# Kernel tuning notes

Hardware: AMD Instinct MI355X
Metric: run time of the kernel (lower is better)

## Reference

```python
import jax, jax.numpy as jnp
import numpy as np
import math

SEQ = 2048      # seq_length_per_batch_item
BATCH = 2
HEADS = 16
HEAD_DIM = 128
SEG_LEN = 1024  # two packed segments per batch item
CAUSAL = True
SCALE = 1.0 / math.sqrt(HEAD_DIM)
MASK_FILL = -10000.0  # matches masked_fill value in torch masked softmax


def setup_inputs() -> dict:
    key = jax.random.key(0)
    k1, k2, k3, k4 = jax.random.split(key, 4)
    query = jax.random.normal(k1, (SEQ, BATCH, HEADS, HEAD_DIM), dtype=jnp.float32)
    key_t = jax.random.normal(k2, (SEQ, BATCH, HEADS, HEAD_DIM), dtype=jnp.float32)
    value = jax.random.normal(k3, (SEQ, BATCH, HEADS, HEAD_DIM), dtype=jnp.float32)
    # additive score manipulation (log-additive branch), broadcast over heads
    score_bias = jax.random.normal(k4, (BATCH, 1, SEQ, SEQ), dtype=jnp.float32) * 0.05
    # packed segment boundaries over the flattened (b*s) token axis;
    # every batch-item boundary (multiple of SEQ) is included, per the torch assert
    cumulative_seq_lengths = jnp.arange(BATCH * SEQ // SEG_LEN + 1, dtype=jnp.int32) * SEG_LEN
    return {
        "query": query,
        "key": key_t,
        "value": value,
        "score_bias": score_bias,
        "cumulative_seq_lengths": cumulative_seq_lengths,
    }


def _dense_mask(cumulative_seq_lengths, batch, seq, causal):
    """Block-diagonal (packed varlen) attention mask.

    Returns bool [b, 1, s, s]; True = masked (disallowed), matching
    cumulative_seq_lengths_to_dense_attention_mask (which returns ~mask).
    """
    # segment id of each token in the flattened (b*s) stream
    flat_pos = jnp.arange(batch * seq, dtype=jnp.int32)
    seg = jnp.searchsorted(cumulative_seq_lengths, flat_pos, side="right")  # [b*s]
    seg = seg.reshape(batch, seq)
    allowed = seg[:, :, None] == seg[:, None, :]  # [b, s, s]
    if causal:
        pos = jnp.arange(seq)
        allowed = allowed & (pos[:, None] >= pos[None, :])
    return ~allowed[:, None, :, :]  # [b, 1, s, s]


def reference(query, key, value, score_bias, cumulative_seq_lengths):
    s, b, n, h = query.shape
    # scores: QK^T scaled -> [b, n, s_q, s_k]
    scores = jnp.einsum("sbnh,tbnh->bnst", query, key) * SCALE
    # additive score manipulation (log-additive branch)
    scores = scores + score_bias
    # block-diagonal varlen mask + causal
    mask = _dense_mask(cumulative_seq_lengths, b, s, CAUSAL)
    scores = jnp.where(mask, MASK_FILL, scores)
    probs = jax.nn.softmax(scores, axis=-1)  # [b, n, s, s]
    # context: probs @ V -> [(b n), s, h], matching torch bmm output layout
    ctx = jnp.einsum("bnst,tbnh->bnsh", probs, value)
    return ctx.reshape(b * n, s, h)
```

## Files before the change

kernel.cpp:

```cpp
#include <hip/hip_runtime.h>
#include <hip/hip_bf16.h>

#define SEQ     2048
#define BATCH   2
#define HEADS   16
#define HD      128
#define SEGL    1024
#define QSCALE  0.08838834764831845f

typedef __attribute__((ext_vector_type(8))) short bf16x8;
typedef __attribute__((ext_vector_type(4))) float f32x4;
typedef unsigned int u32;

__device__ __forceinline__ short f2bf(float f) {
    __hip_bfloat16 h = __float2bfloat16(f);
    return *reinterpret_cast<short*>(&h);
}

__device__ __forceinline__ bf16x8 cvt8(f32x4 x, f32x4 y) {
    bf16x8 t;
    t[0]=f2bf(x[0]); t[1]=f2bf(x[1]); t[2]=f2bf(x[2]); t[3]=f2bf(x[3]);
    t[4]=f2bf(y[0]); t[5]=f2bf(y[1]); t[6]=f2bf(y[2]); t[7]=f2bf(y[3]);
    return t;
}

__device__ __forceinline__ void async16(void* lds, const void* g) {
    __builtin_amdgcn_global_load_lds(
        (const __attribute__((address_space(1))) u32*)g,
        (__attribute__((address_space(3))) u32*)lds, 16, 0, 0);
}

__launch_bounds__(256)
__global__ void prep_kernel(const float* __restrict__ K, const float* __restrict__ V,
                            short* __restrict__ KbfSw, short* __restrict__ VtSw)
{
    const int t  = threadIdx.x;
    const int sT = blockIdx.x;
    const int bh = blockIdx.y;
    const int b  = bh >> 4, h = bh & 15;
    const size_t inBase  = (size_t)sT * 64 * 4096 + (size_t)b * HEADS * HD + (size_t)h * HD;
    const size_t region  = ((size_t)bh * 32 + sT) * 8192;

    if (blockIdx.z == 0) {
        #pragma unroll
        for (int i = 0; i < 4; ++i) {
            const int idx = i * 256 + t;
            const int s_loc = idx >> 4, dg = idx & 15;
            const float* p = K + inBase + (size_t)s_loc * 4096 + dg * 8;
            f32x4 x = *(const f32x4*)p;
            f32x4 y = *(const f32x4*)(p + 4);
            *(bf16x8*)(KbfSw + region + s_loc * 128 + ((dg ^ (s_loc & 7)) * 8)) = cvt8(x, y);
        }
    } else {
        __shared__ __align__(16) short lds[64][136];
        #pragma unroll
        for (int i = 0; i < 4; ++i) {
            const int idx = i * 256 + t;
            const int s_loc = idx >> 4, dg = idx & 15;
            const float* p = V + inBase + (size_t)s_loc * 4096 + dg * 8;
            f32x4 x = *(const f32x4*)p;
            f32x4 y = *(const f32x4*)(p + 4);
            *(bf16x8*)(&lds[s_loc][dg * 8]) = cvt8(x, y);
        }
        __syncthreads();
        const int dp = t & 63;
        const int g  = t >> 6;
        bf16x8 a0, a1, b0_, b1_;
        #pragma unroll
        for (int j = 0; j < 8; ++j) {
            u32 v = *(const u32*)&lds[g * 16 + j][dp * 2];
            a0[j] = (short)(v & 0xffff);
            a1[j] = (short)(v >> 16);
        }
        #pragma unroll
        for (int j = 0; j < 8; ++j) {
            u32 v = *(const u32*)&lds[g * 16 + 8 + j][dp * 2];
            b0_[j] = (short)(v & 0xffff);
            b1_[j] = (short)(v >> 16);
        }
        const int d0c = dp * 2, d1c = dp * 2 + 1;
        short* base0 = VtSw + region + d0c * 64;
        short* base1 = VtSw + region + d1c * 64;
        *(bf16x8*)(base0 + (((g * 2)     ^ (d0c & 7)) * 8)) = a0;
        *(bf16x8*)(base0 + (((g * 2 + 1) ^ (d0c & 7)) * 8)) = b0_;
        *(bf16x8*)(base1 + (((g * 2)     ^ (d1c & 7)) * 8)) = a1;
        *(bf16x8*)(base1 + (((g * 2 + 1) ^ (d1c & 7)) * 8)) = b1_;
    }
}

__launch_bounds__(256, 2)
__global__ void attn_fwd(const float* __restrict__ Q,
                         const short* __restrict__ KbfSw,
                         const short* __restrict__ VtSw,
                         const float* __restrict__ Bias,
                         float* __restrict__ Out)
{
    __shared__ __align__(16) short kbuf[2][8192];
    __shared__ __align__(16) short vbuf[2][8192];
    __shared__ __align__(16) short plds_all[4][16][72];

    const int tid = threadIdx.x;
    const int w   = tid >> 6;
    const int l   = tid & 63;
    const int lo4 = l & 15;
    const int hi4 = l >> 4;
    const int sw  = lo4 & 7;

    const int bsh = blockIdx.x & 63;
    const int st  = 15 - (blockIdx.x >> 6);
    const int h   = bsh & 15;
    const int seg = (bsh >> 4) & 1;
    const int b   = bsh >> 5;
    const int bh  = b * HEADS + h;

    const int segBase = seg * SEGL;
    const int i0  = st * 64 + w * 16;
    const int njt = st + 1;

    short (*plds)[72] = plds_all[w];

    bf16x8 qf[4];
    {
        const float* qp = Q + (size_t)(segBase + i0 + lo4) * 4096
                            + (size_t)b * HEADS * HD + (size_t)h * HD + 8 * hi4;
        #pragma unroll
        for (int c = 0; c < 4; ++c) {
            f32x4 x = *(const f32x4*)(qp + 32 * c);
            f32x4 y = *(const f32x4*)(qp + 32 * c + 4);
            qf[c] = cvt8(x, y);
        }
    }

    f32x4 o[8];
    #pragma unroll
    for (int d = 0; d < 8; ++d) o[d] = (f32x4){0.f, 0.f, 0.f, 0.f};
    float m_run[4] = {-INFINITY, -INFINITY, -INFINITY, -INFINITY};
    float l_run[4] = {0.f, 0.f, 0.f, 0.f};

    const short* kReg = KbfSw + ((size_t)bh * 32 + seg * 16) * 8192;
    const short* vReg = VtSw  + ((size_t)bh * 32 + seg * 16) * 8192;
    const float* bbase = Bias + ((size_t)b * SEQ + segBase) * SEQ + segBase;

    const int ldsOff = w * 2048;
    const int srcOff = w * 2048 + l * 8;

    #pragma unroll
    for (int c = 0; c < 4; ++c) {
        async16(&kbuf[0][ldsOff + c * 512], kReg + srcOff + c * 512);
        async16(&vbuf[0][ldsOff + c * 512], vReg + srcOff + c * 512);
    }
    __syncthreads();

    for (int jt = 0; jt < njt; ++jt) {
        const int cur = jt & 1;
        const int j0  = jt * 64;

        float bv[4][4];
        #pragma unroll
        for (int r = 0; r < 4; ++r) {
            const int qr = i0 + 4 * hi4 + r;
            const float* bp = bbase + (size_t)qr * SEQ + j0;
            #pragma unroll
            for (int ct = 0; ct < 4; ++ct) bv[r][ct] = bp[ct * 16 + lo4];
        }

        if (jt + 1 < njt) {
            const short* kN = kReg + (size_t)(jt + 1) * 8192;
            const short* vN = vReg + (size_t)(jt + 1) * 8192;
            #pragma unroll
            for (int c = 0; c < 4; ++c) {
                async16(&kbuf[cur ^ 1][ldsOff + c * 512], kN + srcOff + c * 512);
                async16(&vbuf[cur ^ 1][ldsOff + c * 512], vN + srcOff + c * 512);
            }
        }

        const short* kb = kbuf[cur];
        const short* vb = vbuf[cur];

        f32x4 s[4];
        #pragma unroll
        for (int ct = 0; ct < 4; ++ct) s[ct] = (f32x4){0.f, 0.f, 0.f, 0.f};
        #pragma unroll
        for (int ct = 0; ct < 4; ++ct) {
            bf16x8 kf[4];
            const short* kr = kb + (ct * 16 + lo4) * 128;
            #pragma unroll
            for (int c = 0; c < 4; ++c)
                kf[c] = *(const bf16x8*)(kr + (((4 * c + hi4) ^ sw) * 8));
            #pragma unroll
            for (int c = 0; c < 4; ++c)
                s[ct] = __builtin_amdgcn_mfma_f32_16x16x32_bf16(qf[c], kf[c], s[ct], 0, 0, 0);
        }

        bf16x8 vfa[8], vfb[8];
        #pragma unroll
        for (int d0 = 0; d0 < 8; ++d0) {
            const short* vr = vb + (d0 * 16 + lo4) * 64;
            vfa[d0] = *(const bf16x8*)(vr + ((hi4 ^ sw) * 8));
            vfb[d0] = *(const bf16x8*)(vr + (((4 + hi4) ^ sw) * 8));
        }

        const bool diag = (jt == njt - 1);
        #pragma unroll
        for (int r = 0; r < 4; ++r) {
            const int qr = i0 + 4 * hi4 + r;
            float v0 = s[0][r] * QSCALE + bv[r][0];
            float v1 = s[1][r] * QSCALE + bv[r][1];
            float v2 = s[2][r] * QSCALE + bv[r][2];
            float v3 = s[3][r] * QSCALE + bv[r][3];
            if (diag) {
                if (j0 + lo4 > qr)      v0 = -INFINITY;
                if (j0 + 16 + lo4 > qr) v1 = -INFINITY;
                if (j0 + 32 + lo4 > qr) v2 = -INFINITY;
                if (j0 + 48 + lo4 > qr) v3 = -INFINITY;
            }
            float mx = fmaxf(fmaxf(v0, v1), fmaxf(v2, v3));
            mx = fmaxf(mx, __shfl_xor(mx, 1));
            mx = fmaxf(mx, __shfl_xor(mx, 2));
            mx = fmaxf(mx, __shfl_xor(mx, 4));
            mx = fmaxf(mx, __shfl_xor(mx, 8));
            const float mnew = fmaxf(m_run[r], mx);
            const float p0 = __expf(v0 - mnew);
            const float p1 = __expf(v1 - mnew);
            const float p2 = __expf(v2 - mnew);
            const float p3 = __expf(v3 - mnew);
            const float sc = __expf(m_run[r] - mnew);
            m_run[r] = mnew;
            float rs = p0 + p1 + p2 + p3;
            rs += __shfl_xor(rs, 1);
            rs += __shfl_xor(rs, 2);
            rs += __shfl_xor(rs, 4);
            rs += __shfl_xor(rs, 8);
            l_run[r] = l_run[r] * sc + rs;
            #pragma unroll
            for (int d = 0; d < 8; ++d) o[d][r] *= sc;

            short* prow = plds[4 * hi4 + r];
            prow[lo4]      = f2bf(p0);
            prow[16 + lo4] = f2bf(p1);
            prow[32 + lo4] = f2bf(p2);
            prow[48 + lo4] = f2bf(p3);
        }

        asm volatile("s_waitcnt lgkmcnt(0)" ::: "memory");
        bf16x8 pf0 = *(const bf16x8*)(&plds[lo4][8 * hi4]);
        bf16x8 pf1 = *(const bf16x8*)(&plds[lo4][32 + 8 * hi4]);

        #pragma unroll
        for (int d0 = 0; d0 < 8; ++d0) {
            o[d0] = __builtin_amdgcn_mfma_f32_16x16x32_bf16(pf0, vfa[d0], o[d0], 0, 0, 0);
            o[d0] = __builtin_amdgcn_mfma_f32_16x16x32_bf16(pf1, vfb[d0], o[d0], 0, 0, 0);
        }

        __syncthreads();
    }

    #pragma unroll
    for (int r = 0; r < 4; ++r) {
        const float inv = 1.0f / l_run[r];
        const int srow = segBase + i0 + 4 * hi4 + r;
        float* op = Out + ((size_t)bh * SEQ + (size_t)srow) * HD + lo4;
        #pragma unroll
        for (int d = 0; d < 8; ++d)
            op[d * 16] = o[d][r] * inv;
    }
}

extern "C" void kernel_launch(void* const* d_in, const int* in_sizes, int n_in,
                              void* d_out, int out_size, void* d_ws, size_t ws_size,
                              hipStream_t stream) {
    const float* Q    = (const float*)d_in[0];
    const float* K    = (const float*)d_in[1];
    const float* V    = (const float*)d_in[2];
    const float* Bias = (const float*)d_in[3];
    float* Out = (float*)d_out;

    short* KbfSw = (short*)d_ws;
    short* VtSw  = (short*)d_ws + (size_t)8388608;

    hipLaunchKernelGGL(prep_kernel, dim3(32, 32, 2), dim3(256), 0, stream, K, V, KbfSw, VtSw);
    hipLaunchKernelGGL(attn_fwd, dim3(1024), dim3(256), 0, stream, Q, KbfSw, VtSw, Bias, Out);
}
```

Measured before the change: 206.1 us.

## Pre-layout K/V into MFMA fragment order and load directly from global

The prep kernel now writes K and transposed V in the exact per-lane MFMA fragment order, so each lane reads its 16-byte operand straight from global/L2 with coalesced accesses. The attention kernel drops the LDS double-buffered async K/V staging and the per-tile block barrier, and raises the occupancy hint from 2 to 3 blocks per SIMD. This removes LDS traffic and synchronisation. In exchange, every wave fetches K/V tiles independently from cache (4x redundant global reads per block) and there is no explicit prefetch, so load latency must be hidden by occupancy.

Measured after the change: 222.0 us. 7.7% more time.

```diff
diff --git a/kernel.cpp b/kernel.cpp
--- a/kernel.cpp
+++ b/kernel.cpp
@@ -24,15 +24,9 @@
     return t;
 }
 
-__device__ __forceinline__ void async16(void* lds, const void* g) {
-    __builtin_amdgcn_global_load_lds(
-        (const __attribute__((address_space(1))) u32*)g,
-        (__attribute__((address_space(3))) u32*)lds, 16, 0, 0);
-}
-
 __launch_bounds__(256)
 __global__ void prep_kernel(const float* __restrict__ K, const float* __restrict__ V,
-                            short* __restrict__ KbfSw, short* __restrict__ VtSw)
+                            short* __restrict__ Kfr, short* __restrict__ Vfr)
 {
     const int t  = threadIdx.x;
     const int sT = blockIdx.x;
@@ -46,10 +40,11 @@
         for (int i = 0; i < 4; ++i) {
             const int idx = i * 256 + t;
             const int s_loc = idx >> 4, dg = idx & 15;
+            const int ct = s_loc >> 4, lo4r = s_loc & 15;
             const float* p = K + inBase + (size_t)s_loc * 4096 + dg * 8;
             f32x4 x = *(const f32x4*)p;
             f32x4 y = *(const f32x4*)(p + 4);
-            *(bf16x8*)(KbfSw + region + s_loc * 128 + ((dg ^ (s_loc & 7)) * 8)) = cvt8(x, y);
+            *(bf16x8*)(Kfr + region + (ct * 16 + dg) * 128 + lo4r * 8) = cvt8(x, y);
         }
     } else {
         __shared__ __align__(16) short lds[64][136];
@@ -78,25 +73,21 @@
             b0_[j] = (short)(v & 0xffff);
             b1_[j] = (short)(v >> 16);
         }
-        const int d0c = dp * 2, d1c = dp * 2 + 1;
-        short* base0 = VtSw + region + d0c * 64;
-        short* base1 = VtSw + region + d1c * 64;
-        *(bf16x8*)(base0 + (((g * 2)     ^ (d0c & 7)) * 8)) = a0;
-        *(bf16x8*)(base0 + (((g * 2 + 1) ^ (d0c & 7)) * 8)) = b0_;
-        *(bf16x8*)(base1 + (((g * 2)     ^ (d1c & 7)) * 8)) = a1;
-        *(bf16x8*)(base1 + (((g * 2 + 1) ^ (d1c & 7)) * 8)) = b1_;
-    }
-}
-
-__launch_bounds__(256, 2)
+        short* rg = Vfr + region;
+        *(bf16x8*)(rg + ((2 * g)     * 128 + 2 * dp)     * 8) = a0;
+        *(bf16x8*)(rg + ((2 * g + 1) * 128 + 2 * dp)     * 8) = b0_;
+        *(bf16x8*)(rg + ((2 * g)     * 128 + 2 * dp + 1) * 8) = a1;
+        *(bf16x8*)(rg + ((2 * g + 1) * 128 + 2 * dp + 1) * 8) = b1_;
+    }
+}
+
+__launch_bounds__(256, 3)
 __global__ void attn_fwd(const float* __restrict__ Q,
-                         const short* __restrict__ KbfSw,
-                         const short* __restrict__ VtSw,
+                         const short* __restrict__ Kfr,
+                         const short* __restrict__ Vfr,
                          const float* __restrict__ Bias,
                          float* __restrict__ Out)
 {
-    __shared__ __align__(16) short kbuf[2][8192];
-    __shared__ __align__(16) short vbuf[2][8192];
     __shared__ __align__(16) short plds_all[4][16][72];
 
     const int tid = threadIdx.x;
@@ -104,7 +95,6 @@
     const int l   = tid & 63;
     const int lo4 = l & 15;
     const int hi4 = l >> 4;
-    const int sw  = lo4 & 7;
 
     const int bsh = blockIdx.x & 63;
     const int st  = 15 - (blockIdx.x >> 6);
@@ -137,23 +127,14 @@
     float m_run[4] = {-INFINITY, -INFINITY, -INFINITY, -INFINITY};
     float l_run[4] = {0.f, 0.f, 0.f, 0.f};
 
-    const short* kReg = KbfSw + ((size_t)bh * 32 + seg * 16) * 8192;
-    const short* vReg = VtSw  + ((size_t)bh * 32 + seg * 16) * 8192;
+    const short* kSeg = Kfr + ((size_t)bh * 32 + seg * 16) * 8192;
+    const short* vSeg = Vfr + ((size_t)bh * 32 + seg * 16) * 8192;
     const float* bbase = Bias + ((size_t)b * SEQ + segBase) * SEQ + segBase;
 
-    const int ldsOff = w * 2048;
-    const int srcOff = w * 2048 + l * 8;
-
-    #pragma unroll
-    for (int c = 0; c < 4; ++c) {
-        async16(&kbuf[0][ldsOff + c * 512], kReg + srcOff + c * 512);
-        async16(&vbuf[0][ldsOff + c * 512], vReg + srcOff + c * 512);
-    }
-    __syncthreads();
-
     for (int jt = 0; jt < njt; ++jt) {
-        const int cur = jt & 1;
-        const int j0  = jt * 64;
+        const int j0 = jt * 64;
+        const short* kReg = kSeg + (size_t)jt * 8192;
+        const short* vReg = vSeg + (size_t)jt * 8192;
 
         float bv[4][4];
         #pragma unroll
@@ -164,40 +145,29 @@
             for (int ct = 0; ct < 4; ++ct) bv[r][ct] = bp[ct * 16 + lo4];
         }
 
-        if (jt + 1 < njt) {
-            const short* kN = kReg + (size_t)(jt + 1) * 8192;
-            const short* vN = vReg + (size_t)(jt + 1) * 8192;
-            #pragma unroll
-            for (int c = 0; c < 4; ++c) {
-                async16(&kbuf[cur ^ 1][ldsOff + c * 512], kN + srcOff + c * 512);
-                async16(&vbuf[cur ^ 1][ldsOff + c * 512], vN + srcOff + c * 512);
-            }
-        }
-
-        const short* kb = kbuf[cur];
-        const short* vb = vbuf[cur];
-
         f32x4 s[4];
         #pragma unroll
         for (int ct = 0; ct < 4; ++ct) s[ct] = (f32x4){0.f, 0.f, 0.f, 0.f};
         #pragma unroll
         for (int ct = 0; ct < 4; ++ct) {
-            bf16x8 kf[4];
-            const short* kr = kb + (ct * 16 + lo4) * 128;
-            #pragma unroll
-            for (int c = 0; c < 4; ++c)
-                kf[c] = *(const bf16x8*)(kr + (((4 * c + hi4) ^ sw) * 8));
-            #pragma unroll
-            for (int c = 0; c < 4; ++c)
-                s[ct] = __builtin_amdgcn_mfma_f32_16x16x32_bf16(qf[c], kf[c], s[ct], 0, 0, 0);
-        }
-
+            const short* kp = kReg + ct * 2048 + hi4 * 128 + lo4 * 8;
+            bf16x8 kf0 = *(const bf16x8*)(kp);
+            bf16x8 kf1 = *(const bf16x8*)(kp + 512);
+            bf16x8 kf2 = *(const bf16x8*)(kp + 1024);
+            bf16x8 kf3 = *(const bf16x8*)(kp + 1536);
+            s[ct] = __builtin_amdgcn_mfma_f32_16x16x32_bf16(qf[0], kf0, s[ct], 0, 0, 0);
+            s[ct] = __builtin_amdgcn_mfma_f32_16x16x32_bf16(qf[1], kf1, s[ct], 0, 0, 0);
+            s[ct] = __builtin_amdgcn_mfma_f32_16x16x32_bf16(qf[2], kf2, s[ct], 0, 0, 0);
+            s[ct] = __builtin_amdgcn_mfma_f32_16x16x32_bf16(qf[3], kf3, s[ct], 0, 0, 0);
+        }
+
+        const short* vpa = vReg + hi4 * 1024 + lo4 * 8;
+        const short* vpb = vReg + (4 + hi4) * 1024 + lo4 * 8;
         bf16x8 vfa[8], vfb[8];
         #pragma unroll
         for (int d0 = 0; d0 < 8; ++d0) {
-            const short* vr = vb + (d0 * 16 + lo4) * 64;
-            vfa[d0] = *(const bf16x8*)(vr + ((hi4 ^ sw) * 8));
-            vfb[d0] = *(const bf16x8*)(vr + (((4 + hi4) ^ sw) * 8));
+            vfa[d0] = *(const bf16x8*)(vpa + d0 * 128);
+            vfb[d0] = *(const bf16x8*)(vpb + d0 * 128);
         }
 
         const bool diag = (jt == njt - 1);
@@ -251,8 +221,6 @@
             o[d0] = __builtin_amdgcn_mfma_f32_16x16x32_bf16(pf0, vfa[d0], o[d0], 0, 0, 0);
             o[d0] = __builtin_amdgcn_mfma_f32_16x16x32_bf16(pf1, vfb[d0], o[d0], 0, 0, 0);
         }
-
-        __syncthreads();
     }
 
     #pragma unroll
@@ -275,9 +243,9 @@
     const float* Bias = (const float*)d_in[3];
     float* Out = (float*)d_out;
 
-    short* KbfSw = (short*)d_ws;
-    short* VtSw  = (short*)d_ws + (size_t)8388608;
-
-    hipLaunchKernelGGL(prep_kernel, dim3(32, 32, 2), dim3(256), 0, stream, K, V, KbfSw, VtSw);
-    hipLaunchKernelGGL(attn_fwd, dim3(1024), dim3(256), 0, stream, Q, KbfSw, VtSw, Bias, Out);
-}
+    short* Kfr = (short*)d_ws;
+    short* Vfr = (short*)d_ws + (size_t)8388608;
+
+    hipLaunchKernelGGL(prep_kernel, dim3(32, 32, 2), dim3(256), 0, stream, K, V, Kfr, Vfr);
+    hipLaunchKernelGGL(attn_fwd, dim3(1024), dim3(256), 0, stream, Q, Kfr, Vfr, Bias, Out);
+}
```

## Load V fragments directly from global in MFMA layout, drop V LDS buffers

Applied to the files above, without the earlier changes.

The prep kernel now writes V transposed into a fragment-ready layout, so the attention kernel loads V operands straight from global memory into registers instead of staging them through double-buffered LDS. This halves LDS use so occupancy can rise to 3 blocks per SM. Bias loads are software-prefetched one tile ahead, and the row-sum shuffle reduction is deferred to the epilogue. In exchange there is more register pressure and V loads are exposed to global latency inside the loop.

New measurement: 332.6 us. 1.61x slower.

```diff
diff --git a/kernel.cpp b/kernel.cpp
--- a/kernel.cpp
+++ b/kernel.cpp
@@ -32,7 +32,7 @@
 
 __launch_bounds__(256)
 __global__ void prep_kernel(const float* __restrict__ K, const float* __restrict__ V,
-                            short* __restrict__ KbfSw, short* __restrict__ VtSw)
+                            short* __restrict__ KbfSw, short* __restrict__ Vfr)
 {
     const int t  = threadIdx.x;
     const int sT = blockIdx.x;
@@ -78,25 +78,22 @@
             b0_[j] = (short)(v & 0xffff);
             b1_[j] = (short)(v >> 16);
         }
-        const int d0c = dp * 2, d1c = dp * 2 + 1;
-        short* base0 = VtSw + region + d0c * 64;
-        short* base1 = VtSw + region + d1c * 64;
-        *(bf16x8*)(base0 + (((g * 2)     ^ (d0c & 7)) * 8)) = a0;
-        *(bf16x8*)(base0 + (((g * 2 + 1) ^ (d0c & 7)) * 8)) = b0_;
-        *(bf16x8*)(base1 + (((g * 2)     ^ (d1c & 7)) * 8)) = a1;
-        *(bf16x8*)(base1 + (((g * 2 + 1) ^ (d1c & 7)) * 8)) = b1_;
-    }
-}
-
-__launch_bounds__(256, 2)
+        short* rg = Vfr + region;
+        *(bf16x8*)(rg + ((2 * g)     * 128 + 2 * dp)     * 8) = a0;
+        *(bf16x8*)(rg + ((2 * g + 1) * 128 + 2 * dp)     * 8) = b0_;
+        *(bf16x8*)(rg + ((2 * g)     * 128 + 2 * dp + 1) * 8) = a1;
+        *(bf16x8*)(rg + ((2 * g + 1) * 128 + 2 * dp + 1) * 8) = b1_;
+    }
+}
+
+__launch_bounds__(256, 3)
 __global__ void attn_fwd(const float* __restrict__ Q,
                          const short* __restrict__ KbfSw,
-                         const short* __restrict__ VtSw,
+                         const short* __restrict__ Vfr,
                          const float* __restrict__ Bias,
                          float* __restrict__ Out)
 {
     __shared__ __align__(16) short kbuf[2][8192];
-    __shared__ __align__(16) short vbuf[2][8192];
     __shared__ __align__(16) short plds_all[4][16][72];
 
     const int tid = threadIdx.x;
@@ -138,76 +135,78 @@
     float l_run[4] = {0.f, 0.f, 0.f, 0.f};
 
     const short* kReg = KbfSw + ((size_t)bh * 32 + seg * 16) * 8192;
-    const short* vReg = VtSw  + ((size_t)bh * 32 + seg * 16) * 8192;
+    const short* vSeg = Vfr  + ((size_t)bh * 32 + seg * 16) * 8192;
     const float* bbase = Bias + ((size_t)b * SEQ + segBase) * SEQ + segBase;
 
     const int ldsOff = w * 2048;
     const int srcOff = w * 2048 + l * 8;
 
     #pragma unroll
-    for (int c = 0; c < 4; ++c) {
+    for (int c = 0; c < 4; ++c)
         async16(&kbuf[0][ldsOff + c * 512], kReg + srcOff + c * 512);
-        async16(&vbuf[0][ldsOff + c * 512], vReg + srcOff + c * 512);
+
+    float bvA[4][4];
+    #pragma unroll
+    for (int r = 0; r < 4; ++r) {
+        const float* bp = bbase + (size_t)(i0 + 4 * hi4 + r) * SEQ;
+        #pragma unroll
+        for (int ct = 0; ct < 4; ++ct) bvA[r][ct] = bp[ct * 16 + lo4];
     }
     __syncthreads();
 
     for (int jt = 0; jt < njt; ++jt) {
         const int cur = jt & 1;
         const int j0  = jt * 64;
-
-        float bv[4][4];
+        const short* vReg = vSeg + (size_t)jt * 8192;
+
+        if (jt + 1 < njt) {
+            const short* kN = kReg + (size_t)(jt + 1) * 8192;
+            #pragma unroll
+            for (int c = 0; c < 4; ++c)
+                async16(&kbuf[cur ^ 1][ldsOff + c * 512], kN + srcOff + c * 512);
+        }
+
+        const short* vpa = vReg + hi4 * 1024 + lo4 * 8;
+        const short* vpb = vReg + (4 + hi4) * 1024 + lo4 * 8;
+        bf16x8 vfa[8], vfb[8];
+        #pragma unroll
+        for (int d0 = 0; d0 < 8; ++d0) vfa[d0] = *(const bf16x8*)(vpa + d0 * 128);
+        #pragma unroll
+        for (int d0 = 0; d0 < 8; ++d0) vfb[d0] = *(const bf16x8*)(vpb + d0 * 128);
+
+        float bvB[4][4];
+        if (jt + 1 < njt) {
+            #pragma unroll
+            for (int r = 0; r < 4; ++r) {
+                const float* bp = bbase + (size_t)(i0 + 4 * hi4 + r) * SEQ + j0 + 64;
+                #pragma unroll
+                for (int ct = 0; ct < 4; ++ct) bvB[r][ct] = bp[ct * 16 + lo4];
+            }
+        }
+
+        f32x4 s[4];
+        #pragma unroll
+        for (int ct = 0; ct < 4; ++ct) s[ct] = (f32x4){0.f, 0.f, 0.f, 0.f};
+        #pragma unroll
+        for (int ct = 0; ct < 4; ++ct) {
+            bf16x8 kf[4];
+            const short* kr = kbuf[cur] + (ct * 16 + lo4) * 128;
+            #pragma unroll
+            for (int c = 0; c < 4; ++c)
+                kf[c] = *(const bf16x8*)(kr + (((4 * c + hi4) ^ sw) * 8));
+            #pragma unroll
+            for (int c = 0; c < 4; ++c)
+                s[ct] = __builtin_amdgcn_mfma_f32_16x16x32_bf16(qf[c], kf[c], s[ct], 0, 0, 0);
+        }
+
+        const bool diag = (jt == njt - 1);
         #pragma unroll
         for (int r = 0; r < 4; ++r) {
             const int qr = i0 + 4 * hi4 + r;
-            const float* bp = bbase + (size_t)qr * SEQ + j0;
-            #pragma unroll
-            for (int ct = 0; ct < 4; ++ct) bv[r][ct] = bp[ct * 16 + lo4];
-        }
-
-        if (jt + 1 < njt) {
-            const short* kN = kReg + (size_t)(jt + 1) * 8192;
-            const short* vN = vReg + (size_t)(jt + 1) * 8192;
-            #pragma unroll
-            for (int c = 0; c < 4; ++c) {
-                async16(&kbuf[cur ^ 1][ldsOff + c * 512], kN + srcOff + c * 512);
-                async16(&vbuf[cur ^ 1][ldsOff + c * 512], vN + srcOff + c * 512);
-            }
-        }
-
-        const short* kb = kbuf[cur];
-        const short* vb = vbuf[cur];
-
-        f32x4 s[4];
-        #pragma unroll
-        for (int ct = 0; ct < 4; ++ct) s[ct] = (f32x4){0.f, 0.f, 0.f, 0.f};
-        #pragma unroll
-        for (int ct = 0; ct < 4; ++ct) {
-            bf16x8 kf[4];
-            const short* kr = kb + (ct * 16 + lo4) * 128;
-            #pragma unroll
-            for (int c = 0; c < 4; ++c)
-                kf[c] = *(const bf16x8*)(kr + (((4 * c + hi4) ^ sw) * 8));
-            #pragma unroll
-            for (int c = 0; c < 4; ++c)
-                s[ct] = __builtin_amdgcn_mfma_f32_16x16x32_bf16(qf[c], kf[c], s[ct], 0, 0, 0);
-        }
-
-        bf16x8 vfa[8], vfb[8];
-        #pragma unroll
-        for (int d0 = 0; d0 < 8; ++d0) {
-            const short* vr = vb + (d0 * 16 + lo4) * 64;
-            vfa[d0] = *(const bf16x8*)(vr + ((hi4 ^ sw) * 8));
-            vfb[d0] = *(const bf16x8*)(vr + (((4 + hi4) ^ sw) * 8));
-        }
-
-        const bool diag = (jt == njt - 1);
-        #pragma unroll
-        for (int r = 0; r < 4; ++r) {
-            const int qr = i0 + 4 * hi4 + r;
-            float v0 = s[0][r] * QSCALE + bv[r][0];
-            float v1 = s[1][r] * QSCALE + bv[r][1];
-            float v2 = s[2][r] * QSCALE + bv[r][2];
-            float v3 = s[3][r] * QSCALE + bv[r][3];
+            float v0 = s[0][r] * QSCALE + bvA[r][0];
+            float v1 = s[1][r] * QSCALE + bvA[r][1];
+            float v2 = s[2][r] * QSCALE + bvA[r][2];
+            float v3 = s[3][r] * QSCALE + bvA[r][3];
             if (diag) {
                 if (j0 + lo4 > qr)      v0 = -INFINITY;
                 if (j0 + 16 + lo4 > qr) v1 = -INFINITY;
@@ -226,12 +225,7 @@
             const float p3 = __expf(v3 - mnew);
             const float sc = __expf(m_run[r] - mnew);
             m_run[r] = mnew;
-            float rs = p0 + p1 + p2 + p3;
-            rs += __shfl_xor(rs, 1);
-            rs += __shfl_xor(rs, 2);
-            rs += __shfl_xor(rs, 4);
-            rs += __shfl_xor(rs, 8);
-            l_run[r] = l_run[r] * sc + rs;
+            l_run[r] = l_run[r] * sc + (p0 + p1 + p2 + p3);
             #pragma unroll
             for (int d = 0; d < 8; ++d) o[d][r] *= sc;
 
@@ -247,9 +241,17 @@
         bf16x8 pf1 = *(const bf16x8*)(&plds[lo4][32 + 8 * hi4]);
 
         #pragma unroll
-        for (int d0 = 0; d0 < 8; ++d0) {
+        for (int d0 = 0; d0 < 8; ++d0)
             o[d0] = __builtin_amdgcn_mfma_f32_16x16x32_bf16(pf0, vfa[d0], o[d0], 0, 0, 0);
+        #pragma unroll
+        for (int d0 = 0; d0 < 8; ++d0)
             o[d0] = __builtin_amdgcn_mfma_f32_16x16x32_bf16(pf1, vfb[d0], o[d0], 0, 0, 0);
+
+        if (jt + 1 < njt) {
+            #pragma unroll
+            for (int r = 0; r < 4; ++r)
+                #pragma unroll
+                for (int ct = 0; ct < 4; ++ct) bvA[r][ct] = bvB[r][ct];
         }
 
         __syncthreads();
@@ -257,7 +259,12 @@
 
     #pragma unroll
     for (int r = 0; r < 4; ++r) {
-        const float inv = 1.0f / l_run[r];
+        float rs = l_run[r];
+        rs += __shfl_xor(rs, 1);
+        rs += __shfl_xor(rs, 2);
+        rs += __shfl_xor(rs, 4);
+        rs += __shfl_xor(rs, 8);
+        const float inv = 1.0f / rs;
         const int srow = segBase + i0 + 4 * hi4 + r;
         float* op = Out + ((size_t)bh * SEQ + (size_t)srow) * HD + lo4;
         #pragma unroll
@@ -276,8 +283,8 @@
     float* Out = (float*)d_out;
 
     short* KbfSw = (short*)d_ws;
-    short* VtSw  = (short*)d_ws + (size_t)8388608;
-
-    hipLaunchKernelGGL(prep_kernel, dim3(32, 32, 2), dim3(256), 0, stream, K, V, KbfSw, VtSw);
-    hipLaunchKernelGGL(attn_fwd, dim3(1024), dim3(256), 0, stream, Q, KbfSw, VtSw, Bias, Out);
-}
+    short* Vfr   = (short*)d_ws + (size_t)8388608;
+
+    hipLaunchKernelGGL(prep_kernel, dim3(32, 32, 2), dim3(256), 0, stream, K, V, KbfSw, Vfr);
+    hipLaunchKernelGGL(attn_fwd, dim3(1024), dim3(256), 0, stream, Q, KbfSw, Vfr, Bias, Out);
+}
```

## Prefetch bias one tile ahead, split barriers, defer row-sum reduction

Applied to the files above, without the earlier changes.

Bias values for the next key tile are loaded one iteration ahead into registers, so global-load latency overlaps with the current tile's compute. The single __syncthreads at loop end becomes explicit s_barrier and vmcnt waits placed around the async K/V prefetch. The per-iteration cross-lane row-sum shuffles are removed: each lane keeps a partial l and the reduction runs once at the end, which is valid because the rescale factor is uniform across the row. The cost is more registers for the second bias buffer, plus fragile hand-written vmcnt counts that interact with the bias loads.

Measured after the change: 208.7 us. No clear change (+1.3%).

```diff
diff --git a/kernel.cpp b/kernel.cpp
--- a/kernel.cpp
+++ b/kernel.cpp
@@ -149,22 +149,22 @@
         async16(&kbuf[0][ldsOff + c * 512], kReg + srcOff + c * 512);
         async16(&vbuf[0][ldsOff + c * 512], vReg + srcOff + c * 512);
     }
+    float bvA[4][4];
+    #pragma unroll
+    for (int r = 0; r < 4; ++r) {
+        const float* bp = bbase + (size_t)(i0 + 4 * hi4 + r) * SEQ;
+        #pragma unroll
+        for (int ct = 0; ct < 4; ++ct) bvA[r][ct] = bp[ct * 16 + lo4];
+    }
     __syncthreads();
 
     for (int jt = 0; jt < njt; ++jt) {
         const int cur = jt & 1;
         const int j0  = jt * 64;
-
-        float bv[4][4];
-        #pragma unroll
-        for (int r = 0; r < 4; ++r) {
-            const int qr = i0 + 4 * hi4 + r;
-            const float* bp = bbase + (size_t)qr * SEQ + j0;
-            #pragma unroll
-            for (int ct = 0; ct < 4; ++ct) bv[r][ct] = bp[ct * 16 + lo4];
-        }
-
-        if (jt + 1 < njt) {
+        const bool more = (jt + 1 < njt);
+
+        if (more) {
+            asm volatile("s_barrier" ::: "memory");
             const short* kN = kReg + (size_t)(jt + 1) * 8192;
             const short* vN = vReg + (size_t)(jt + 1) * 8192;
             #pragma unroll
@@ -172,10 +172,21 @@
                 async16(&kbuf[cur ^ 1][ldsOff + c * 512], kN + srcOff + c * 512);
                 async16(&vbuf[cur ^ 1][ldsOff + c * 512], vN + srcOff + c * 512);
             }
-        }
-
-        const short* kb = kbuf[cur];
-        const short* vb = vbuf[cur];
+            asm volatile("s_waitcnt vmcnt(8)" ::: "memory");
+        } else {
+            asm volatile("s_waitcnt vmcnt(0)" ::: "memory");
+        }
+        asm volatile("s_barrier" ::: "memory");
+
+        float bvB[4][4];
+        if (more) {
+            #pragma unroll
+            for (int r = 0; r < 4; ++r) {
+                const float* bp = bbase + (size_t)(i0 + 4 * hi4 + r) * SEQ + j0 + 64;
+                #pragma unroll
+                for (int ct = 0; ct < 4; ++ct) bvB[r][ct] = bp[ct * 16 + lo4];
+            }
+        }
 
         f32x4 s[4];
         #pragma unroll
@@ -183,7 +194,7 @@
         #pragma unroll
         for (int ct = 0; ct < 4; ++ct) {
             bf16x8 kf[4];
-            const short* kr = kb + (ct * 16 + lo4) * 128;
+            const short* kr = kbuf[cur] + (ct * 16 + lo4) * 128;
             #pragma unroll
             for (int c = 0; c < 4; ++c)
                 kf[c] = *(const bf16x8*)(kr + (((4 * c + hi4) ^ sw) * 8));
@@ -195,7 +206,7 @@
         bf16x8 vfa[8], vfb[8];
         #pragma unroll
         for (int d0 = 0; d0 < 8; ++d0) {
-            const short* vr = vb + (d0 * 16 + lo4) * 64;
+            const short* vr = vbuf[cur] + (d0 * 16 + lo4) * 64;
             vfa[d0] = *(const bf16x8*)(vr + ((hi4 ^ sw) * 8));
             vfb[d0] = *(const bf16x8*)(vr + (((4 + hi4) ^ sw) * 8));
         }
@@ -204,10 +215,10 @@
         #pragma unroll
         for (int r = 0; r < 4; ++r) {
             const int qr = i0 + 4 * hi4 + r;
-            float v0 = s[0][r] * QSCALE + bv[r][0];
-            float v1 = s[1][r] * QSCALE + bv[r][1];
-            float v2 = s[2][r] * QSCALE + bv[r][2];
-            float v3 = s[3][r] * QSCALE + bv[r][3];
+            float v0 = s[0][r] * QSCALE + bvA[r][0];
+            float v1 = s[1][r] * QSCALE + bvA[r][1];
+            float v2 = s[2][r] * QSCALE + bvA[r][2];
+            float v3 = s[3][r] * QSCALE + bvA[r][3];
             if (diag) {
                 if (j0 + lo4 > qr)      v0 = -INFINITY;
                 if (j0 + 16 + lo4 > qr) v1 = -INFINITY;
@@ -226,12 +237,7 @@
             const float p3 = __expf(v3 - mnew);
             const float sc = __expf(m_run[r] - mnew);
             m_run[r] = mnew;
-            float rs = p0 + p1 + p2 + p3;
-            rs += __shfl_xor(rs, 1);
-            rs += __shfl_xor(rs, 2);
-            rs += __shfl_xor(rs, 4);
-            rs += __shfl_xor(rs, 8);
-            l_run[r] = l_run[r] * sc + rs;
+            l_run[r] = l_run[r] * sc + (p0 + p1 + p2 + p3);
             #pragma unroll
             for (int d = 0; d < 8; ++d) o[d][r] *= sc;
 
@@ -252,12 +258,22 @@
             o[d0] = __builtin_amdgcn_mfma_f32_16x16x32_bf16(pf1, vfb[d0], o[d0], 0, 0, 0);
         }
 
-        __syncthreads();
+        if (more) {
+            #pragma unroll
+            for (int r = 0; r < 4; ++r)
+                #pragma unroll
+                for (int ct = 0; ct < 4; ++ct) bvA[r][ct] = bvB[r][ct];
+        }
     }
 
     #pragma unroll
     for (int r = 0; r < 4; ++r) {
-        const float inv = 1.0f / l_run[r];
+        float rs = l_run[r];
+        rs += __shfl_xor(rs, 1);
+        rs += __shfl_xor(rs, 2);
+        rs += __shfl_xor(rs, 4);
+        rs += __shfl_xor(rs, 8);
+        const float inv = 1.0f / rs;
         const int srow = segBase + i0 + 4 * hi4 + r;
         float* op = Out + ((size_t)bh * SEQ + (size_t)srow) * HD + lo4;
         #pragma unroll
```
